# Kernel tuning notes

Measured on AMD Instinct MI355X. Metric: run time of the kernel, lower is better.

## Reference

```python
import jax, jax.numpy as jnp
import numpy as np

HEIGHT = 8  # init kwarg: output crop height
B, J, C, HIMG, WIMG = 8, 64, 32, 256, 256


def _make_boxes():
    rng = np.random.default_rng(0)
    left = rng.uniform(0.0, 40.0, (B, J))
    bw = rng.uniform(16.0, 200.0, (B, J))
    top = rng.uniform(0.0, 200.0, (B, J))
    bh = rng.uniform(8.0, 32.0, (B, J))
    theta = rng.uniform(-0.5, 0.5, (B, J))  # unused by the original forward
    return np.stack([left, top, left + bw, top + bh, theta], axis=-1).astype(np.float32)


def _box_widths(boxes_np):
    # torch: width = int(aspect * height), truncation (values are positive)
    bw = boxes_np[..., 2] - boxes_np[..., 0]
    bh = boxes_np[..., 3] - boxes_np[..., 1]
    return ((bw / bh) * HEIGHT).astype(np.int32)  # [B, J]


def setup_inputs() -> dict:
    key = jax.random.key(0)
    image = jax.random.normal(key, (B, C, HIMG, WIMG), dtype=jnp.float32)
    boxes = jnp.asarray(_make_boxes())
    return {"image": image, "boxes": boxes}


def reference(image, boxes):
    # Per-box widths are integer (shape-determining) constants, taken from concrete box data.
    boxes_np = np.asarray(jax.device_get(boxes))
    widths_np = _box_widths(boxes_np)          # [B, J] ints >= 2
    max_w = int(widths_np.max())
    widths = jnp.asarray(widths_np)

    dt = boxes.dtype
    base_w = boxes[..., 2] - boxes[..., 0]      # [B, J]
    base_h = boxes[..., 3] - boxes[..., 1]
    each_w = base_w / (widths.astype(dt) - 1)   # [B, J]
    each_h = base_h / (HEIGHT - 1)

    # Sampling grids: xx [B,J,Wm], yy [B,J,Hh]
    xx = jnp.arange(max_w, dtype=dt)[None, None, :] * each_w[..., None] + boxes[..., 0:1]
    yy = jnp.arange(HEIGHT, dtype=dt)[None, None, :] * each_h[..., None] + boxes[..., 1:2]

    def interp_one_image(img, x, y):
        # img [C,Hi,Wi], x [J,Wm], y [J,Hh] -> [C,J,Hh,Wm]
        x0 = jnp.clip(jnp.floor(x).astype(jnp.int32), 0, WIMG - 1)
        x1 = jnp.clip(jnp.floor(x).astype(jnp.int32) + 1, 0, WIMG - 1)
        y0 = jnp.clip(jnp.floor(y).astype(jnp.int32), 0, HIMG - 1)
        y1 = jnp.clip(jnp.floor(y).astype(jnp.int32) + 1, 0, HIMG - 1)
        # gathers: [C, J, Hh, Wm]
        ia = img[:, y0[:, :, None], x0[:, None, :]]
        ib = img[:, y1[:, :, None], x0[:, None, :]]
        ic = img[:, y0[:, :, None], x1[:, None, :]]
        idd = img[:, y1[:, :, None], x1[:, None, :]]
        x0f, x1f = x0.astype(dt), x1.astype(dt)
        y0f, y1f = y0.astype(dt), y1.astype(dt)
        wa = (x1f - x)[:, None, :] * (y1f - y)[:, :, None]  # [J,Hh,Wm]
        wb = (x1f - x)[:, None, :] * (y - y0f)[:, :, None]
        wc = (x - x0f)[:, None, :] * (y1f - y)[:, :, None]
        wd = (x - x0f)[:, None, :] * (y - y0f)[:, :, None]
        return ia * wa[None] + ib * wb[None] + ic * wc[None] + idd * wd[None]

    res = jax.vmap(interp_one_image)(image, xx, yy)      # [B,C,J,Hh,Wm]
    res = jnp.transpose(res, (0, 2, 1, 3, 4))            # [B,J,C,Hh,Wm]

    mask = (jnp.arange(max_w)[None, None, :] < widths[..., None]).astype(jnp.uint8)  # [B,J,Wm]
    res = res * mask[:, :, None, None, :].astype(res.dtype)  # zero-pad beyond each box width
    return res, mask
```

## Files before the change

### kernel.cpp

```cpp
#include <hip/hip_runtime.h>

#define HIMG 256
#define WIMG 256
#define CCH  32
#define JBOX 64
#define BIMG 8
#define HGT  8

__global__ __launch_bounds__(256) void roi_kernel(
    const float* __restrict__ img,
    const float* __restrict__ boxes,
    float* __restrict__ res,
    float* __restrict__ mask,
    int max_w)
{
    const int blk = blockIdx.x;
    const int h   = blk & 7;
    const int bj  = blk >> 3;
    const int b   = bj >> 6;
    const int i   = threadIdx.x;

    const float left = boxes[bj * 5 + 0];
    const float top  = boxes[bj * 5 + 1];
    const float bw   = boxes[bj * 5 + 2] - left;
    const float bh   = boxes[bj * 5 + 3] - top;

    const int   width  = (int)(bw / bh * 8.0f);
    const float each_w = bw / ((float)width - 1.0f);
    const float each_h = bh / 7.0f;

    if (i >= max_w) return;
    const bool in_w = (i < width);

    if (h == 0) {
        __builtin_nontemporal_store(in_w ? 1.0f : 0.0f,
                                    &mask[(size_t)bj * max_w + i]);
    }

    float* resp = res + ((size_t)bj * CCH * HGT + h) * (size_t)max_w + i;
    const size_t c_stride = (size_t)HGT * max_w;

    if (!in_w) {
        #pragma unroll
        for (int c = 0; c < CCH; ++c) {
            __builtin_nontemporal_store(0.0f, &resp[(size_t)c * c_stride]);
        }
        return;
    }

    const float x = __fadd_rn(__fmul_rn((float)i, each_w), left);
    const float y = __fadd_rn(__fmul_rn((float)h, each_h), top);

    const int xf = (int)floorf(x);
    const int yf = (int)floorf(y);
    const int x0 = min(max(xf,     0), WIMG - 1);
    const int x1 = min(max(xf + 1, 0), WIMG - 1);
    const int y0 = min(max(yf,     0), HIMG - 1);
    const int y1 = min(max(yf + 1, 0), HIMG - 1);

    const float wx1 = (float)x1 - x;
    const float wx0 = x - (float)x0;
    const float wy1 = (float)y1 - y;
    const float wy0 = y - (float)y0;

    const float wa = wx1 * wy1;
    const float wb = wx1 * wy0;
    const float wc = wx0 * wy1;
    const float wd = wx0 * wy0;

    const size_t img_base = (size_t)b * CCH * HIMG * WIMG;
    const int o00 = y0 * WIMG + x0;
    const int o10 = y1 * WIMG + x0;
    const int o01 = y0 * WIMG + x1;
    const int o11 = y1 * WIMG + x1;

    #pragma unroll 8
    for (int c = 0; c < CCH; ++c) {
        const float* im = img + img_base + (size_t)c * (HIMG * WIMG);
        const float va = im[o00];
        const float vb = im[o10];
        const float vc = im[o01];
        const float vd = im[o11];
        const float val = va * wa + vb * wb + vc * wc + vd * wd;
        __builtin_nontemporal_store(val, &resp[(size_t)c * c_stride]);
    }
}

extern "C" void kernel_launch(void* const* d_in, const int* in_sizes, int n_in,
                              void* d_out, int out_size, void* d_ws, size_t ws_size,
                              hipStream_t stream) {
    const float* img   = (const float*)d_in[0];
    const float* boxes = (const float*)d_in[1];
    float* out = (float*)d_out;

    const int per_w = BIMG * JBOX * CCH * HGT + BIMG * JBOX;
    const int max_w = out_size / per_w;

    float* res  = out;
    float* mask = out + (size_t)BIMG * JBOX * CCH * HGT * max_w;

    const int blocks = BIMG * JBOX * HGT;
    roi_kernel<<<blocks, 256, 0, stream>>>(img, boxes, res, mask, max_w);
}
```

Baseline: 184.9 us.

## Stage the two needed image rows per channel in shared memory before interpolating

Each block now uses coalesced loads to copy the two source rows (y0, y1) of all 32 channels, over the box's horizontal span, into shared memory. The bilinear taps are then read from LDS instead of being scattered global gathers. This is meant to replace uncoalesced per-thread global loads with contiguous row loads. In exchange, each block uses about 52 KB of LDS, which limits occupancy, and it may read pixels that are never sampled. The fixed LMAX of 204 assumes box spans stay within that size; wider boxes would write past the shared-memory rows.

```diff
diff --git a/kernel.cpp b/kernel.cpp
--- a/kernel.cpp
+++ b/kernel.cpp
@@ -6,6 +6,7 @@
 #define JBOX 64
 #define BIMG 8
 #define HGT  8
+#define LMAX 204
 
 __global__ __launch_bounds__(256) void roi_kernel(
     const float* __restrict__ img,
@@ -14,25 +15,55 @@
     float* __restrict__ mask,
     int max_w)
 {
+    __shared__ float smem[CCH][2][LMAX];
+
     const int blk = blockIdx.x;
     const int h   = blk & 7;
     const int bj  = blk >> 3;
     const int b   = bj >> 6;
-    const int i   = threadIdx.x;
+    const int tid = threadIdx.x;
 
-    const float left = boxes[bj * 5 + 0];
-    const float top  = boxes[bj * 5 + 1];
-    const float bw   = boxes[bj * 5 + 2] - left;
-    const float bh   = boxes[bj * 5 + 3] - top;
+    const float left  = boxes[bj * 5 + 0];
+    const float top   = boxes[bj * 5 + 1];
+    const float right = boxes[bj * 5 + 2];
+    const float bot   = boxes[bj * 5 + 3];
+    const float bw = right - left;
+    const float bh = bot - top;
 
     const int   width  = (int)(bw / bh * 8.0f);
     const float each_w = bw / ((float)width - 1.0f);
     const float each_h = bh / 7.0f;
 
-    if (i >= max_w) return;
+    const float y  = __fadd_rn(__fmul_rn((float)h, each_h), top);
+    const int   yf = (int)floorf(y);
+    const int   y0 = min(max(yf,     0), HIMG - 1);
+    const int   y1 = min(max(yf + 1, 0), HIMG - 1);
+    const float wy1 = (float)y1 - y;
+    const float wy0 = y - (float)y0;
+
+    const int xs = max((int)floorf(left), 0);
+    const int xe = min((int)floorf(right) + 2, WIMG - 1);
+    const int L  = xe - xs + 1;
+
+    {
+        const int g    = tid >> 5;
+        const int lane = tid & 31;
+        for (int seg = g; seg < 2 * CCH; seg += 8) {
+            const int ch  = seg >> 1;
+            const int r   = seg & 1;
+            const int row = r ? y1 : y0;
+            const float* src = img + (((size_t)b * CCH + ch) * HIMG + row) * WIMG;
+            for (int off = lane; off < L; off += 32) {
+                smem[ch][r][off] = src[xs + off];
+            }
+        }
+    }
+
+    const int  i    = tid;
+    const bool have = (i < max_w);
     const bool in_w = (i < width);
 
-    if (h == 0) {
+    if (h == 0 && have) {
         __builtin_nontemporal_store(in_w ? 1.0f : 0.0f,
                                     &mask[(size_t)bj * max_w + i]);
     }
@@ -40,49 +71,40 @@
     float* resp = res + ((size_t)bj * CCH * HGT + h) * (size_t)max_w + i;
     const size_t c_stride = (size_t)HGT * max_w;
 
-    if (!in_w) {
+    if (have && !in_w) {
         #pragma unroll
         for (int c = 0; c < CCH; ++c) {
             __builtin_nontemporal_store(0.0f, &resp[(size_t)c * c_stride]);
         }
-        return;
     }
 
-    const float x = __fadd_rn(__fmul_rn((float)i, each_w), left);
-    const float y = __fadd_rn(__fmul_rn((float)h, each_h), top);
+    __syncthreads();
 
-    const int xf = (int)floorf(x);
-    const int yf = (int)floorf(y);
-    const int x0 = min(max(xf,     0), WIMG - 1);
-    const int x1 = min(max(xf + 1, 0), WIMG - 1);
-    const int y0 = min(max(yf,     0), HIMG - 1);
-    const int y1 = min(max(yf + 1, 0), HIMG - 1);
+    if (have && in_w) {
+        const float x  = __fadd_rn(__fmul_rn((float)i, each_w), left);
+        const int   xf = (int)floorf(x);
+        const int   x0 = min(max(xf,     0), WIMG - 1);
+        const int   x1 = min(max(xf + 1, 0), WIMG - 1);
 
-    const float wx1 = (float)x1 - x;
-    const float wx0 = x - (float)x0;
-    const float wy1 = (float)y1 - y;
-    const float wy0 = y - (float)y0;
+        const float wx1 = (float)x1 - x;
+        const float wx0 = x - (float)x0;
+        const float wa = wx1 * wy1;
+        const float wb = wx1 * wy0;
+        const float wc = wx0 * wy1;
+        const float wd = wx0 * wy0;
 
-    const float wa = wx1 * wy1;
-    const float wb = wx1 * wy0;
-    const float wc = wx0 * wy1;
-    const float wd = wx0 * wy0;
+        const int lx0 = min(max(x0 - xs, 0), LMAX - 1);
+        const int lx1 = min(max(x1 - xs, 0), LMAX - 1);
 
-    const size_t img_base = (size_t)b * CCH * HIMG * WIMG;
-    const int o00 = y0 * WIMG + x0;
-    const int o10 = y1 * WIMG + x0;
-    const int o01 = y0 * WIMG + x1;
-    const int o11 = y1 * WIMG + x1;
-
-    #pragma unroll 8
-    for (int c = 0; c < CCH; ++c) {
-        const float* im = img + img_base + (size_t)c * (HIMG * WIMG);
-        const float va = im[o00];
-        const float vb = im[o10];
-        const float vc = im[o01];
-        const float vd = im[o11];
-        const float val = va * wa + vb * wb + vc * wc + vd * wd;
-        __builtin_nontemporal_store(val, &resp[(size_t)c * c_stride]);
+        #pragma unroll 8
+        for (int c = 0; c < CCH; ++c) {
+            const float va = smem[c][0][lx0];
+            const float vc = smem[c][0][lx1];
+            const float vb = smem[c][1][lx0];
+            const float vd = smem[c][1][lx1];
+            const float val = va * wa + vb * wb + vc * wc + vd * wd;
+            __builtin_nontemporal_store(val, &resp[(size_t)c * c_stride]);
+        }
     }
 }
 
```

Result: slower. 195.2 us (+5.6%).

## Split channels across wavefronts and tile width in 64-lane tiles

Applied to the files above, without the earlier changes.

Each 256-thread block now covers 64 output columns, with each of its four wavefronts handling 8 of the 32 channels, instead of one thread per column looping over all channels. The grid gains a second dimension over width tiles, so threads past max_w are no longer wasted when max_w is below 256, and each thread has fewer serial gathers. Stores switch from nontemporal to ordinary writes. The cost is more blocks, and the box parameters are recomputed in every wavefront.

```diff
diff --git a/kernel.cpp b/kernel.cpp
--- a/kernel.cpp
+++ b/kernel.cpp
@@ -6,6 +6,7 @@
 #define JBOX 64
 #define BIMG 8
 #define HGT  8
+#define CPW  8
 
 __global__ __launch_bounds__(256) void roi_kernel(
     const float* __restrict__ img,
@@ -14,11 +15,14 @@
     float* __restrict__ mask,
     int max_w)
 {
-    const int blk = blockIdx.x;
-    const int h   = blk & 7;
-    const int bj  = blk >> 3;
-    const int b   = bj >> 6;
-    const int i   = threadIdx.x;
+    const int tile = blockIdx.x;
+    const int bjh  = blockIdx.y;
+    const int h    = bjh & 7;
+    const int bj   = bjh >> 3;
+    const int b    = bj >> 6;
+    const int wv   = threadIdx.x >> 6;
+    const int lane = threadIdx.x & 63;
+    const int i    = tile * 64 + lane;
 
     const float left = boxes[bj * 5 + 0];
     const float top  = boxes[bj * 5 + 1];
@@ -32,18 +36,17 @@
     if (i >= max_w) return;
     const bool in_w = (i < width);
 
-    if (h == 0) {
-        __builtin_nontemporal_store(in_w ? 1.0f : 0.0f,
-                                    &mask[(size_t)bj * max_w + i]);
+    if (h == 0 && wv == 0) {
+        mask[(size_t)bj * max_w + i] = in_w ? 1.0f : 0.0f;
     }
 
-    float* resp = res + ((size_t)bj * CCH * HGT + h) * (size_t)max_w + i;
+    float* resp = res + (((size_t)bj * CCH + wv * CPW) * HGT + h) * (size_t)max_w + i;
     const size_t c_stride = (size_t)HGT * max_w;
 
     if (!in_w) {
         #pragma unroll
-        for (int c = 0; c < CCH; ++c) {
-            __builtin_nontemporal_store(0.0f, &resp[(size_t)c * c_stride]);
+        for (int c = 0; c < CPW; ++c) {
+            resp[(size_t)c * c_stride] = 0.0f;
         }
         return;
     }
@@ -68,21 +71,21 @@
     const float wc = wx0 * wy1;
     const float wd = wx0 * wy0;
 
-    const size_t img_base = (size_t)b * CCH * HIMG * WIMG;
+    const float* im = img + ((size_t)b * CCH + wv * CPW) * (HIMG * WIMG);
     const int o00 = y0 * WIMG + x0;
     const int o10 = y1 * WIMG + x0;
     const int o01 = y0 * WIMG + x1;
     const int o11 = y1 * WIMG + x1;
 
-    #pragma unroll 8
-    for (int c = 0; c < CCH; ++c) {
-        const float* im = img + img_base + (size_t)c * (HIMG * WIMG);
-        const float va = im[o00];
-        const float vb = im[o10];
-        const float vc = im[o01];
-        const float vd = im[o11];
+    #pragma unroll
+    for (int c = 0; c < CPW; ++c) {
+        const float* imc = im + (size_t)c * (HIMG * WIMG);
+        const float va = imc[o00];
+        const float vb = imc[o10];
+        const float vc = imc[o01];
+        const float vd = imc[o11];
         const float val = va * wa + vb * wb + vc * wc + vd * wd;
-        __builtin_nontemporal_store(val, &resp[(size_t)c * c_stride]);
+        resp[(size_t)c * c_stride] = val;
     }
 }
 
@@ -99,6 +102,7 @@
     float* res  = out;
     float* mask = out + (size_t)BIMG * JBOX * CCH * HGT * max_w;
 
-    const int blocks = BIMG * JBOX * HGT;
-    roi_kernel<<<blocks, 256, 0, stream>>>(img, boxes, res, mask, max_w);
+    const int tiles = (max_w + 63) / 64;
+    dim3 grid(tiles, BIMG * JBOX * HGT);
+    roi_kernel<<<grid, 256, 0, stream>>>(img, boxes, res, mask, max_w);
 }
```

Result: faster. 154.1 us (-16.6%).
